# Kernel tuning notes

Measured on AMD Instinct MI355X. Metric: run time of the kernel, lower is better.

## Reference

```python
import jax, jax.numpy as jnp
import numpy as np

B, S, H = 1, 2048, 1024   # batch, seq_len, hidden_size
E, K, I = 8, 2, 1024      # num_experts, top_k, intermediate_size


def setup_inputs() -> dict:
    key = jax.random.key(0)
    ks = jax.random.split(key, 5)
    x = jax.random.normal(ks[0], (B, S, H), dtype=jnp.float32)
    gate_w = jax.random.normal(ks[1], (H, E), dtype=jnp.float32) * 0.02
    wg = jax.random.normal(ks[2], (E, H, I), dtype=jnp.float32) * 0.02  # gate_proj per expert
    wu = jax.random.normal(ks[3], (E, H, I), dtype=jnp.float32) * 0.02  # up_proj per expert
    wd = jax.random.normal(ks[4], (E, I, H), dtype=jnp.float32) * 0.02  # down_proj per expert
    return {"x": x, "gate_w": gate_w, "wg": wg, "wu": wu, "wd": wd}


def _moe(x, gate_w, wg, wu, wd):
    b, s, h = x.shape
    n = b * s
    logits = jnp.einsum('bsh,he->bse', x, gate_w)          # [B,S,E]
    top_vals, sel = jax.lax.top_k(logits, K)               # [B,S,K]
    rweights = jax.nn.softmax(top_vals, axis=-1)           # [B,S,K]
    x_flat = x.reshape(n, h)
    sel_flat = sel.reshape(n, K)
    rw_flat = rweights.reshape(n, K)

    def expert_body(out, params):
        e, Wg, Wu, Wd = params
        hit = jnp.any(sel_flat == e, axis=-1)              # [N] tokens routed to e in any slot
        # stable argsort: hit tokens first, in ascending original index order
        perm = jnp.argsort(jnp.logical_not(hit))
        tokens = x_flat[perm]                              # [N,H] (row j = j-th token of token_indices)
        y = jnp.einsum('ni,ih->nh', jax.nn.silu(tokens @ Wg) * (tokens @ Wu), Wd)  # [N,H]
        contrib = jnp.zeros_like(out)
        for k in range(K):
            km = sel_flat[:, k] == e                       # [N]
            # original does output_flat[k_indices] += w * expert_output[:len(k_indices)]
            # i.e. j-th token of k_indices gets expert_output row j
            ranks = jnp.clip(jnp.cumsum(km) - 1, 0, n - 1)
            w = jnp.where(km, rw_flat[:, k], 0.0)
            contrib = contrib + w[:, None] * y[ranks]
        return out + contrib, None

    out, _ = jax.lax.scan(expert_body, jnp.zeros_like(x_flat),
                          (jnp.arange(E), wg, wu, wd))
    output = out.reshape(b, s, h)

    # aux metrics (match LoadBalancedRouter)
    probs = jax.nn.softmax(logits, axis=-1)
    usage = probs.mean(axis=(0, 1))                        # [E]
    balance_loss = jnp.var(usage, ddof=1) * E              # torch.var is unbiased
    su = jnp.sort(usage)
    idx = jnp.arange(1, E + 1, dtype=usage.dtype)
    gini = 2.0 * (idx * su).sum() / (E * su.sum()) - (E + 1.0) / E
    entropy = -(probs * jnp.log(probs + 1e-10)).sum(-1).mean()
    return output, balance_loss, gini, entropy


def reference(x, gate_w, wg, wu, wd):
    return _moe(x, gate_w, wg, wu, wd)
```

## Files before the change

kernel.cpp:

```cpp
#include <hip/hip_runtime.h>
#include <stdint.h>

#define TOKENS 2048
#define HID 1024
#define NE 8

typedef __attribute__((ext_vector_type(8))) short bf16x8;
typedef __attribute__((ext_vector_type(4))) float f32x4;

__device__ __forceinline__ unsigned short f2bf(float f) {
  unsigned int u = __float_as_uint(f);
  return (unsigned short)((u + 0x7fffu + ((u >> 16) & 1u)) >> 16);
}

__device__ __forceinline__ void gload16(const void* g, void* l) {
  __builtin_amdgcn_global_load_lds((const __attribute__((address_space(1))) void*)g,
                                   (__attribute__((address_space(3))) void*)l, 16, 0, 0);
}

__global__ __launch_bounds__(256) void k_rout(
    const float* __restrict__ x, const float* __restrict__ gw,
    int* __restrict__ sel, float* __restrict__ rw,
    float* __restrict__ probs, float* __restrict__ ent) {
  const int w = threadIdx.x >> 6;
  const int lane = threadIdx.x & 63;
  const int t = blockIdx.x * 4 + w;

  const float4* x4 = (const float4*)(x + (size_t)t * HID);
  const float4* gw4 = (const float4*)gw;

  float acc[NE];
#pragma unroll
  for (int e = 0; e < NE; ++e) acc[e] = 0.f;

#pragma unroll
  for (int i = 0; i < 4; ++i) {
    const int idx4 = i * 64 + lane;
    const float4 xv = x4[idx4];
    float4 g[8];
#pragma unroll
    for (int k = 0; k < 8; ++k) g[k] = gw4[(size_t)idx4 * 8 + k];
    const float xs[4] = {xv.x, xv.y, xv.z, xv.w};
#pragma unroll
    for (int c = 0; c < 4; ++c) {
      acc[0] += xs[c] * g[c * 2].x;
      acc[1] += xs[c] * g[c * 2].y;
      acc[2] += xs[c] * g[c * 2].z;
      acc[3] += xs[c] * g[c * 2].w;
      acc[4] += xs[c] * g[c * 2 + 1].x;
      acc[5] += xs[c] * g[c * 2 + 1].y;
      acc[6] += xs[c] * g[c * 2 + 1].z;
      acc[7] += xs[c] * g[c * 2 + 1].w;
    }
  }

#pragma unroll
  for (int e = 0; e < NE; ++e) {
#pragma unroll
    for (int msk = 32; msk >= 1; msk >>= 1) acc[e] += __shfl_xor(acc[e], msk, 64);
  }

  float mx = acc[0];
#pragma unroll
  for (int e = 1; e < NE; ++e) mx = fmaxf(mx, acc[e]);

  const int e8 = lane & 7;
  float my = acc[0];
#pragma unroll
  for (int k = 1; k < NE; ++k) if (e8 == k) my = acc[k];
  const float exl = expf(my - mx);
  float S = exl;
#pragma unroll
  for (int msk = 1; msk <= 4; msk <<= 1) S += __shfl_xor(S, msk, 64);
  const float pp = exl / S;
  if (lane < 8) probs[t * NE + lane] = pp;
  float ev = -pp * logf(pp + 1e-10f);
#pragma unroll
  for (int msk = 1; msk <= 4; msk <<= 1) ev += __shfl_xor(ev, msk, 64);

  if (lane == 0) {
    ent[t] = ev;
    int b0 = 0; float v0 = acc[0];
#pragma unroll
    for (int e = 1; e < NE; ++e) if (acc[e] > v0) { v0 = acc[e]; b0 = e; }
    int b1 = -1; float v1 = 0.f;
#pragma unroll
    for (int e = 0; e < NE; ++e) {
      if (e != b0 && (b1 < 0 || acc[e] > v1)) { v1 = acc[e]; b1 = e; }
    }
    const float w1e = expf(v1 - v0);
    const float s2 = 1.f + w1e;
    sel[t * 2] = b0; sel[t * 2 + 1] = b1;
    rw[t * 2] = 1.f / s2; rw[t * 2 + 1] = w1e / s2;
  }
}

__global__ void k_metrics(const float* __restrict__ probs, const float* __restrict__ ent,
                          float* __restrict__ dout) {
  __shared__ float red[256][NE];
  __shared__ float rede[256];
  const int tid = threadIdx.x;
  const float4* p4 = (const float4*)probs;
  float pa[NE];
#pragma unroll
  for (int e = 0; e < NE; ++e) pa[e] = 0.f;
  float ea = 0.f;
  for (int t = tid; t < TOKENS; t += 256) {
    const float4 a = p4[t * 2];
    const float4 b = p4[t * 2 + 1];
    pa[0] += a.x; pa[1] += a.y; pa[2] += a.z; pa[3] += a.w;
    pa[4] += b.x; pa[5] += b.y; pa[6] += b.z; pa[7] += b.w;
    ea += ent[t];
  }
#pragma unroll
  for (int e = 0; e < NE; ++e) red[tid][e] = pa[e];
  rede[tid] = ea;
  __syncthreads();
  for (int s = 128; s >= 1; s >>= 1) {
    if (tid < s) {
#pragma unroll
      for (int e = 0; e < NE; ++e) red[tid][e] += red[tid + s][e];
      rede[tid] += rede[tid + s];
    }
    __syncthreads();
  }
  if (tid == 0) {
    float us[NE];
    for (int e = 0; e < NE; ++e) us[e] = red[0][e] / (float)TOKENS;
    float mean = 0.f;
    for (int e = 0; e < NE; ++e) mean += us[e];
    mean /= (float)NE;
    float var = 0.f;
    for (int e = 0; e < NE; ++e) { const float d = us[e] - mean; var += d * d; }
    var /= (float)(NE - 1);
    const float bl = var * (float)NE;
    for (int i = 1; i < NE; ++i) {
      const float key = us[i]; int j = i - 1;
      while (j >= 0 && us[j] > key) { us[j + 1] = us[j]; --j; }
      us[j + 1] = key;
    }
    float num = 0.f, den = 0.f;
    for (int i = 0; i < NE; ++i) { num += (float)(i + 1) * us[i]; den += us[i]; }
    const float gini = 2.f * num / ((float)NE * den) - (float)(NE + 1) / (float)NE;
    dout[(size_t)TOKENS * HID] = bl;
    dout[(size_t)TOKENS * HID + 1] = gini;
    dout[(size_t)TOKENS * HID + 2] = rede[0] / (float)TOKENS;
  }
}

__global__ void k_lists(const int* __restrict__ sel, int* __restrict__ cnt,
                        int* __restrict__ hit_list, int* __restrict__ rowidx) {
  const int e = blockIdx.x;
  const int tid = threadIdx.x;
  __shared__ unsigned long long ssum[256];
  __shared__ unsigned long long csumA[256];
  __shared__ unsigned long long csumB[256];

  int s0[8], s1[8];
  unsigned long long mine = 0ull;
  unsigned long long cA = 0ull, cB = 0ull;
#pragma unroll
  for (int j = 0; j < 8; ++j) {
    const int t = tid * 8 + j;
    s0[j] = sel[2 * t]; s1[j] = sel[2 * t + 1];
#pragma unroll
    for (int q = 0; q < 4; ++q) {
      cA += ((unsigned long long)((s0[j] == q) + (s1[j] == q))) << (16 * q);
      cB += ((unsigned long long)((s0[j] == q + 4) + (s1[j] == q + 4))) << (16 * q);
    }
    const unsigned long long k0 = (s0[j] == e) ? 1ull : 0ull;
    const unsigned long long k1 = (s1[j] == e) ? 1ull : 0ull;
    mine += (k0 | k1) | (k0 << 21) | (k1 << 42);
  }
  ssum[tid] = mine;
  csumA[tid] = cA;
  csumB[tid] = cB;
  __syncthreads();
  for (int s = 128; s >= 1; s >>= 1) {
    if (tid < s) { csumA[tid] += csumA[tid + s]; csumB[tid] += csumB[tid + s]; }
    __syncthreads();
  }
  const unsigned long long totA = csumA[0];
  const unsigned long long totB = csumB[0];
  int tc[NE];
#pragma unroll
  for (int q = 0; q < 4; ++q) {
    tc[q] = (int)((totA >> (16 * q)) & 0xFFFFull);
    tc[q + 4] = (int)((totB >> (16 * q)) & 0xFFFFull);
  }
  if (e == 0 && tid < NE) cnt[tid] = tc[tid];
  int poff = 0;
#pragma unroll
  for (int q = 0; q < NE; ++q) if (q < e) poff += (tc[q] + 127) & ~127;

  for (int s = 1; s < 256; s <<= 1) {
    const unsigned long long v = (tid >= s) ? ssum[tid - s] : 0ull;
    __syncthreads();
    ssum[tid] += v;
    __syncthreads();
  }
  const unsigned long long excl = (tid > 0) ? ssum[tid - 1] : 0ull;
  int hc = (int)(excl & 0x1FFFFFull);
  int c0 = (int)((excl >> 21) & 0x1FFFFFull);
  int c1 = (int)((excl >> 42) & 0x1FFFFFull);
#pragma unroll
  for (int j = 0; j < 8; ++j) {
    const int t = tid * 8 + j;
    const int k0 = (s0[j] == e), k1 = (s1[j] == e);
    if (k0 | k1) { hit_list[poff + hc] = t; ++hc; }
    if (k0) { rowidx[2 * t] = poff + c0; ++c0; }
    if (k1) { rowidx[2 * t + 1] = poff + c1; ++c1; }
  }
}

__global__ void k_tw(const float* __restrict__ wg, const float* __restrict__ wu,
                     const float* __restrict__ wd, unsigned short* __restrict__ wgt,
                     unsigned short* __restrict__ wut, unsigned short* __restrict__ wdt) {
  __shared__ float tile[64][65];
  const int bx = blockIdx.x;
  const int by = blockIdx.y;
  const int mi = blockIdx.z;
  const int tensor = mi >> 3, e = mi & 7;
  const float* src = (tensor == 0 ? wg : tensor == 1 ? wu : wd) + ((size_t)e << 20);
  unsigned short* dst = (tensor == 0 ? wgt : tensor == 1 ? wut : wdt) + ((size_t)e << 20);
  const int tid = threadIdx.x;
  const int tr = tid >> 4, tc = (tid & 15) * 4;
#pragma unroll
  for (int p = 0; p < 4; ++p) {
    const int row = p * 16 + tr;
    const float4 v = *(const float4*)(src + (size_t)(by * 64 + row) * 1024 + bx * 64 + tc);
    tile[row][tc] = v.x; tile[row][tc + 1] = v.y; tile[row][tc + 2] = v.z; tile[row][tc + 3] = v.w;
  }
  __syncthreads();
#pragma unroll
  for (int p = 0; p < 4; ++p) {
    const int row = p * 16 + tr;
    const ushort4 o = make_ushort4(f2bf(tile[tc + 0][row]), f2bf(tile[tc + 1][row]),
                                   f2bf(tile[tc + 2][row]), f2bf(tile[tc + 3][row]));
    *(ushort4*)(dst + (size_t)(bx * 64 + row) * 1024 + by * 64 + tc) = o;
  }
}

__global__ void k_gather(const float* __restrict__ x, const int* __restrict__ hit_list,
                         const int* __restrict__ cnt, unsigned short* __restrict__ A) {
  const int mb = blockIdx.x, e = blockIdx.y;
  const int ce = cnt[e];
  const int pc = (ce + 127) & ~127;
  if (mb * 8 >= pc) return;
  int poff = 0;
  for (int q = 0; q < e; ++q) poff += (cnt[q] + 127) & ~127;
  const int tid = threadIdx.x;
#pragma unroll
  for (int i = 0; i < 8; ++i) {
    const int rr = mb * 8 + i;
    unsigned short* dst = A + (size_t)(poff + rr) * 1024 + tid * 4;
    if (rr < ce) {
      const int t = hit_list[poff + rr];
      const float4 v = *(const float4*)(x + (size_t)t * 1024 + tid * 4);
      *(ushort4*)dst = make_ushort4(f2bf(v.x), f2bf(v.y), f2bf(v.z), f2bf(v.w));
    } else {
      *(ushort4*)dst = make_ushort4(0, 0, 0, 0);
    }
  }
}

__global__ __launch_bounds__(256, 4) void k_gemm1(
    const unsigned short* __restrict__ A, const unsigned short* __restrict__ wgt,
    const unsigned short* __restrict__ wut, const int* __restrict__ cnt,
    unsigned short* __restrict__ T) {
  const int nb = blockIdx.x, mb = blockIdx.y, e = blockIdx.z;
  const int ce = cnt[e];
  if (mb * 128 >= ce) return;
  int poff = 0;
  for (int q = 0; q < e; ++q) poff += (cnt[q] + 127) & ~127;

  const unsigned short* Ab = A + (size_t)(poff + mb * 128) * 1024;
  const unsigned short* Bg = wgt + ((size_t)e << 20) + ((size_t)nb << 16);
  const unsigned short* Bu = wut + ((size_t)e << 20) + ((size_t)nb << 16);

  __shared__ __align__(16) short lds[3][8192];

  const int tid = threadIdx.x;
  const int lane = tid & 63;
  const int w = tid >> 6;
  const int wm = w & 1, wn = w >> 1;
  const int r = lane & 15, gq = lane >> 4;
  const int slot = gq ^ ((r >> 1) & 3);
  const int srow = lane >> 2;
  const int skoff = ((lane & 3) ^ ((lane >> 3) & 3)) << 3;

  f32x4 accg[4][2], accu[4][2];
  const f32x4 fz = {0.f, 0.f, 0.f, 0.f};
#pragma unroll
  for (int i = 0; i < 4; ++i)
#pragma unroll
    for (int j = 0; j < 2; ++j) { accg[i][j] = fz; accu[i][j] = fz; }

  auto stage = [&](int kt, int b) {
#pragma unroll
    for (int q = 0; q < 4; ++q) {
      const int gseg = w + q * 4;
      const unsigned short* sb;
      int seg;
      if (gseg < 8) { sb = Ab; seg = gseg; }
      else if (gseg < 12) { sb = Bg; seg = gseg - 8; }
      else { sb = Bu; seg = gseg - 12; }
      gload16(sb + (size_t)(seg * 16 + srow) * 1024 + kt * 32 + skoff,
              &lds[b][gseg * 512]);
    }
  };

  stage(0, 0); stage(1, 1); stage(2, 2);
  int curb = 0;
  for (int kt = 0; kt < 32; ++kt) {
    if (kt < 30)      { asm volatile("s_waitcnt vmcnt(8)" ::: "memory"); }
    else if (kt == 30){ asm volatile("s_waitcnt vmcnt(4)" ::: "memory"); }
    else              { asm volatile("s_waitcnt vmcnt(0)" ::: "memory"); }
    __builtin_amdgcn_sched_barrier(0);
    __builtin_amdgcn_s_barrier();
    __builtin_amdgcn_sched_barrier(0);

    const short* La = &lds[curb][0];
    const short* Lg = &lds[curb][4096];
    const short* Lu = &lds[curb][6144];
    bf16x8 af[4], gf[2], uf[2];
#pragma unroll
    for (int f = 0; f < 4; ++f)
      af[f] = *(const bf16x8*)(La + (wm * 64 + f * 16 + r) * 32 + slot * 8);
#pragma unroll
    for (int f = 0; f < 2; ++f) {
      gf[f] = *(const bf16x8*)(Lg + (wn * 32 + f * 16 + r) * 32 + slot * 8);
      uf[f] = *(const bf16x8*)(Lu + (wn * 32 + f * 16 + r) * 32 + slot * 8);
    }
    asm volatile("s_waitcnt lgkmcnt(0)" ::: "memory");
    __builtin_amdgcn_sched_barrier(0);
    __builtin_amdgcn_s_barrier();
    __builtin_amdgcn_sched_barrier(0);
    if (kt <= 28) stage(kt + 3, curb);

#pragma unroll
    for (int i = 0; i < 4; ++i)
#pragma unroll
      for (int j = 0; j < 2; ++j) {
        accg[i][j] = __builtin_amdgcn_mfma_f32_16x16x32_bf16(af[i], gf[j], accg[i][j], 0, 0, 0);
        accu[i][j] = __builtin_amdgcn_mfma_f32_16x16x32_bf16(af[i], uf[j], accu[i][j], 0, 0, 0);
      }
    curb = (curb == 2) ? 0 : curb + 1;
  }

  const size_t rowbase = (size_t)(poff + mb * 128);
#pragma unroll
  for (int i = 0; i < 4; ++i)
#pragma unroll
    for (int j = 0; j < 2; ++j) {
      const int col = nb * 64 + wn * 32 + j * 16 + r;
#pragma unroll
      for (int rr = 0; rr < 4; ++rr) {
        const int rowt = wm * 64 + i * 16 + gq * 4 + rr;
        const float gv = accg[i][j][rr];
        const float uv = accu[i][j][rr];
        const float sv = gv / (1.f + expf(-gv)) * uv;
        T[(rowbase + rowt) * 1024 + col] = f2bf(sv);
      }
    }
}

__global__ __launch_bounds__(256, 4) void k_gemm2(
    const unsigned short* __restrict__ T, const unsigned short* __restrict__ wdt,
    const int* __restrict__ cnt, float* __restrict__ Y) {
  const int nb = blockIdx.x, mb = blockIdx.y, e = blockIdx.z;
  const int ce = cnt[e];
  if (mb * 128 >= ce) return;
  int poff = 0;
  for (int q = 0; q < e; ++q) poff += (cnt[q] + 127) & ~127;

  const unsigned short* Ab = T + (size_t)(poff + mb * 128) * 1024;
  const unsigned short* Bd = wdt + ((size_t)e << 20) + ((size_t)nb << 16);

  __shared__ __align__(16) short lds[3][6144];

  const int tid = threadIdx.x;
  const int lane = tid & 63;
  const int w = tid >> 6;
  const int wm = w & 1, wn = w >> 1;
  const int r = lane & 15, gq = lane >> 4;
  const int slot = gq ^ ((r >> 1) & 3);
  const int srow = lane >> 2;
  const int skoff = ((lane & 3) ^ ((lane >> 3) & 3)) << 3;

  f32x4 acc[4][2];
  const f32x4 fz = {0.f, 0.f, 0.f, 0.f};
#pragma unroll
  for (int i = 0; i < 4; ++i)
#pragma unroll
    for (int j = 0; j < 2; ++j) acc[i][j] = fz;

  auto stage = [&](int kt, int b) {
#pragma unroll
    for (int q = 0; q < 3; ++q) {
      const int gseg = w + q * 4;
      const unsigned short* sb;
      int seg;
      if (gseg < 8) { sb = Ab; seg = gseg; }
      else { sb = Bd; seg = gseg - 8; }
      gload16(sb + (size_t)(seg * 16 + srow) * 1024 + kt * 32 + skoff,
              &lds[b][gseg * 512]);
    }
  };

  stage(0, 0); stage(1, 1); stage(2, 2);
  int curb = 0;
  for (int kt = 0; kt < 32; ++kt) {
    if (kt < 30)      { asm volatile("s_waitcnt vmcnt(6)" ::: "memory"); }
    else if (kt == 30){ asm volatile("s_waitcnt vmcnt(3)" ::: "memory"); }
    else              { asm volatile("s_waitcnt vmcnt(0)" ::: "memory"); }
    __builtin_amdgcn_sched_barrier(0);
    __builtin_amdgcn_s_barrier();
    __builtin_amdgcn_sched_barrier(0);

    const short* La = &lds[curb][0];
    const short* Lb = &lds[curb][4096];
    bf16x8 af[4], bfr[2];
#pragma unroll
    for (int f = 0; f < 4; ++f)
      af[f] = *(const bf16x8*)(La + (wm * 64 + f * 16 + r) * 32 + slot * 8);
#pragma unroll
    for (int f = 0; f < 2; ++f)
      bfr[f] = *(const bf16x8*)(Lb + (wn * 32 + f * 16 + r) * 32 + slot * 8);
    asm volatile("s_waitcnt lgkmcnt(0)" ::: "memory");
    __builtin_amdgcn_sched_barrier(0);
    __builtin_amdgcn_s_barrier();
    __builtin_amdgcn_sched_barrier(0);
    if (kt <= 28) stage(kt + 3, curb);

#pragma unroll
    for (int i = 0; i < 4; ++i)
#pragma unroll
      for (int j = 0; j < 2; ++j)
        acc[i][j] = __builtin_amdgcn_mfma_f32_16x16x32_bf16(af[i], bfr[j], acc[i][j], 0, 0, 0);
    curb = (curb == 2) ? 0 : curb + 1;
  }

  const size_t rowbase = (size_t)(poff + mb * 128);
#pragma unroll
  for (int i = 0; i < 4; ++i)
#pragma unroll
    for (int j = 0; j < 2; ++j) {
      const int col = nb * 64 + wn * 32 + j * 16 + r;
#pragma unroll
      for (int rr = 0; rr < 4; ++rr) {
        const int rowt = wm * 64 + i * 16 + gq * 4 + rr;
        Y[(rowbase + rowt) * 1024 + col] = acc[i][j][rr];
      }
    }
}

__global__ void k_out(const float* __restrict__ Y, const int* __restrict__ rowidx,
                      const float* __restrict__ rw, float* __restrict__ out) {
  const int t = blockIdx.x;
  const int tid = threadIdx.x;
  const int r0 = rowidx[2 * t], r1 = rowidx[2 * t + 1];
  const float w0 = rw[2 * t], w1 = rw[2 * t + 1];
  const float4 y0 = *(const float4*)(Y + (size_t)r0 * HID + tid * 4);
  const float4 y1 = *(const float4*)(Y + (size_t)r1 * HID + tid * 4);
  float4 o;
  o.x = w0 * y0.x + w1 * y1.x;
  o.y = w0 * y0.y + w1 * y1.y;
  o.z = w0 * y0.z + w1 * y1.z;
  o.w = w0 * y0.w + w1 * y1.w;
  *(float4*)(out + (size_t)t * HID + tid * 4) = o;
}

extern "C" void kernel_launch(void* const* d_in, const int* in_sizes, int n_in,
                              void* d_out, int out_size, void* d_ws, size_t ws_size,
                              hipStream_t stream) {
  const float* x = (const float*)d_in[0];
  const float* gw = (const float*)d_in[1];
  const float* wg = (const float*)d_in[2];
  const float* wu = (const float*)d_in[3];
  const float* wd = (const float*)d_in[4];
  float* out = (float*)d_out;

  char* p = (char*)d_ws;
  unsigned short* wgt = (unsigned short*)p;
  unsigned short* wut = (unsigned short*)(p + 16777216);
  float* Y = (float*)p;
  unsigned short* wdt = (unsigned short*)(p + 33554432);
  unsigned short* A = (unsigned short*)(p + 50331648);
  unsigned short* T = (unsigned short*)(p + 60817408);
  char* q = p + 71303168;
  float* probs = (float*)q; q += 65536;
  float* ent = (float*)q; q += 8192;
  int* sel = (int*)q; q += 16384;
  float* rwp = (float*)q; q += 16384;
  int* rowidx = (int*)q; q += 16384;
  int* hit_list = (int*)q; q += 20480;
  int* cnt = (int*)q;

  k_rout<<<512, 256, 0, stream>>>(x, gw, sel, rwp, probs, ent);
  k_lists<<<8, 256, 0, stream>>>(sel, cnt, hit_list, rowidx);
  k_metrics<<<1, 256, 0, stream>>>(probs, ent, out);
  k_tw<<<dim3(16, 16, 24), 256, 0, stream>>>(wg, wu, wd, wgt, wut, wdt);
  k_gather<<<dim3(256, 8), 256, 0, stream>>>(x, hit_list, cnt, A);
  k_gemm1<<<dim3(16, 16, 8), 256, 0, stream>>>(A, wgt, wut, cnt, T);
  k_gemm2<<<dim3(16, 16, 8), 256, 0, stream>>>(T, wdt, cnt, Y);
  k_out<<<2048, 256, 0, stream>>>(Y, rowidx, rwp, out);
}
```

Before: 127.1 us.

## Fuse weight transpose and bf16 conversion into expert GEMM loaders

```diff
diff --git a/kernel.cpp b/kernel.cpp
--- a/kernel.cpp
+++ b/kernel.cpp
@@ -213,34 +213,6 @@
   }
 }
 
-__global__ void k_tw(const float* __restrict__ wg, const float* __restrict__ wu,
-                     const float* __restrict__ wd, unsigned short* __restrict__ wgt,
-                     unsigned short* __restrict__ wut, unsigned short* __restrict__ wdt) {
-  __shared__ float tile[64][65];
-  const int bx = blockIdx.x;
-  const int by = blockIdx.y;
-  const int mi = blockIdx.z;
-  const int tensor = mi >> 3, e = mi & 7;
-  const float* src = (tensor == 0 ? wg : tensor == 1 ? wu : wd) + ((size_t)e << 20);
-  unsigned short* dst = (tensor == 0 ? wgt : tensor == 1 ? wut : wdt) + ((size_t)e << 20);
-  const int tid = threadIdx.x;
-  const int tr = tid >> 4, tc = (tid & 15) * 4;
-#pragma unroll
-  for (int p = 0; p < 4; ++p) {
-    const int row = p * 16 + tr;
-    const float4 v = *(const float4*)(src + (size_t)(by * 64 + row) * 1024 + bx * 64 + tc);
-    tile[row][tc] = v.x; tile[row][tc + 1] = v.y; tile[row][tc + 2] = v.z; tile[row][tc + 3] = v.w;
-  }
-  __syncthreads();
-#pragma unroll
-  for (int p = 0; p < 4; ++p) {
-    const int row = p * 16 + tr;
-    const ushort4 o = make_ushort4(f2bf(tile[tc + 0][row]), f2bf(tile[tc + 1][row]),
-                                   f2bf(tile[tc + 2][row]), f2bf(tile[tc + 3][row]));
-    *(ushort4*)(dst + (size_t)(bx * 64 + row) * 1024 + by * 64 + tc) = o;
-  }
-}
-
 __global__ void k_gather(const float* __restrict__ x, const int* __restrict__ hit_list,
                          const int* __restrict__ cnt, unsigned short* __restrict__ A) {
   const int mb = blockIdx.x, e = blockIdx.y;
@@ -264,9 +236,9 @@
   }
 }
 
-__global__ __launch_bounds__(256, 4) void k_gemm1(
-    const unsigned short* __restrict__ A, const unsigned short* __restrict__ wgt,
-    const unsigned short* __restrict__ wut, const int* __restrict__ cnt,
+__global__ __launch_bounds__(256, 3) void k_gemm1(
+    const unsigned short* __restrict__ A, const float* __restrict__ wg,
+    const float* __restrict__ wu, const int* __restrict__ cnt,
     unsigned short* __restrict__ T) {
   const int nb = blockIdx.x, mb = blockIdx.y, e = blockIdx.z;
   const int ce = cnt[e];
@@ -275,8 +247,8 @@
   for (int q = 0; q < e; ++q) poff += (cnt[q] + 127) & ~127;
 
   const unsigned short* Ab = A + (size_t)(poff + mb * 128) * 1024;
-  const unsigned short* Bg = wgt + ((size_t)e << 20) + ((size_t)nb << 16);
-  const unsigned short* Bu = wut + ((size_t)e << 20) + ((size_t)nb << 16);
+  const float* Wg = wg + ((size_t)e << 20) + nb * 64;
+  const float* Wu = wu + ((size_t)e << 20) + nb * 64;
 
   __shared__ __align__(16) short lds[3][8192];
 
@@ -285,9 +257,11 @@
   const int w = tid >> 6;
   const int wm = w & 1, wn = w >> 1;
   const int r = lane & 15, gq = lane >> 4;
-  const int slot = gq ^ ((r >> 1) & 3);
+  const int aslot = gq ^ ((r >> 1) & 3);
+  const int wslot = gq ^ ((r >> 2) & 3);
   const int srow = lane >> 2;
   const int skoff = ((lane & 3) ^ ((lane >> 3) & 3)) << 3;
+  const int kp = tid >> 4, n4i = tid & 15;
 
   f32x4 accg[4][2], accu[4][2];
   const f32x4 fz = {0.f, 0.f, 0.f, 0.f};
@@ -296,48 +270,75 @@
 #pragma unroll
     for (int j = 0; j < 2; ++j) { accg[i][j] = fz; accu[i][j] = fz; }
 
-  auto stage = [&](int kt, int b) {
-#pragma unroll
-    for (int q = 0; q < 4; ++q) {
-      const int gseg = w + q * 4;
-      const unsigned short* sb;
-      int seg;
-      if (gseg < 8) { sb = Ab; seg = gseg; }
-      else if (gseg < 12) { sb = Bg; seg = gseg - 8; }
-      else { sb = Bu; seg = gseg - 12; }
-      gload16(sb + (size_t)(seg * 16 + srow) * 1024 + kt * 32 + skoff,
-              &lds[b][gseg * 512]);
-    }
-  };
-
-  stage(0, 0); stage(1, 1); stage(2, 2);
-  int curb = 0;
-  for (int kt = 0; kt < 32; ++kt) {
-    if (kt < 30)      { asm volatile("s_waitcnt vmcnt(8)" ::: "memory"); }
-    else if (kt == 30){ asm volatile("s_waitcnt vmcnt(4)" ::: "memory"); }
-    else              { asm volatile("s_waitcnt vmcnt(0)" ::: "memory"); }
-    __builtin_amdgcn_sched_barrier(0);
-    __builtin_amdgcn_s_barrier();
-    __builtin_amdgcn_sched_barrier(0);
-
+  auto stageA = [&](int kt, int b) {
+#pragma unroll
+    for (int q = 0; q < 2; ++q) {
+      const int seg = w + q * 4;
+      gload16(Ab + (size_t)(seg * 16 + srow) * 1024 + kt * 32 + skoff,
+              &lds[b][seg * 512]);
+    }
+  };
+  auto wload = [&](const float* W, int kt, float4& r0, float4& r1) {
+    const float* s = W + (size_t)(kt * 32 + 2 * kp) * 1024 + 4 * n4i;
+    r0 = *(const float4*)s;
+    r1 = *(const float4*)(s + 1024);
+  };
+  auto wwrite = [&](int b, int base, const float4& lo, const float4& hi) {
+    short* Lw = &lds[b][base];
+    const float l4[4] = {lo.x, lo.y, lo.z, lo.w};
+    const float h4[4] = {hi.x, hi.y, hi.z, hi.w};
+#pragma unroll
+    for (int j = 0; j < 4; ++j) {
+      unsigned int pk;
+      asm("v_cvt_pk_bf16_f32 %0, %1, %2" : "=v"(pk) : "v"(l4[j]), "v"(h4[j]));
+      const int n = 4 * n4i + j;
+      const int ps = (kp >> 2) ^ (n4i & 3);
+      *(unsigned int*)(Lw + n * 32 + ps * 8 + (kp & 3) * 2) = pk;
+    }
+  };
+
+  stageA(0, 0); stageA(1, 1); stageA(2, 2);
+  float4 g0A, g1A, u0A, u1A, g0B, g1B, u0B, u1B;
+  wload(Wg, 0, g0A, g1A); wload(Wu, 0, u0A, u1A);
+  wload(Wg, 1, g0B, g1B); wload(Wu, 1, u0B, u1B);
+  wwrite(0, 4096, g0A, g1A); wwrite(0, 6144, u0A, u1A);
+  wload(Wg, 2, g0A, g1A); wload(Wu, 2, u0A, u1A);
+  wwrite(1, 4096, g0B, g1B); wwrite(1, 6144, u0B, u1B);
+  asm volatile("s_waitcnt lgkmcnt(0)" ::: "memory");
+
+  auto iter = [&](int kt, float4& lg0, float4& lg1, float4& lu0, float4& lu1,
+                  const float4& sg0, const float4& sg1, const float4& su0, const float4& su1) {
+    asm volatile("s_waitcnt vmcnt(12)" ::: "memory");
+    __builtin_amdgcn_sched_barrier(0);
+    __builtin_amdgcn_s_barrier();
+    __builtin_amdgcn_sched_barrier(0);
+    const int curb = kt % 3;
     const short* La = &lds[curb][0];
     const short* Lg = &lds[curb][4096];
     const short* Lu = &lds[curb][6144];
     bf16x8 af[4], gf[2], uf[2];
 #pragma unroll
     for (int f = 0; f < 4; ++f)
-      af[f] = *(const bf16x8*)(La + (wm * 64 + f * 16 + r) * 32 + slot * 8);
+      af[f] = *(const bf16x8*)(La + (wm * 64 + f * 16 + r) * 32 + aslot * 8);
 #pragma unroll
     for (int f = 0; f < 2; ++f) {
-      gf[f] = *(const bf16x8*)(Lg + (wn * 32 + f * 16 + r) * 32 + slot * 8);
-      uf[f] = *(const bf16x8*)(Lu + (wn * 32 + f * 16 + r) * 32 + slot * 8);
+      gf[f] = *(const bf16x8*)(Lg + (wn * 32 + f * 16 + r) * 32 + wslot * 8);
+      uf[f] = *(const bf16x8*)(Lu + (wn * 32 + f * 16 + r) * 32 + wslot * 8);
     }
     asm volatile("s_waitcnt lgkmcnt(0)" ::: "memory");
     __builtin_amdgcn_sched_barrier(0);
     __builtin_amdgcn_s_barrier();
     __builtin_amdgcn_sched_barrier(0);
-    if (kt <= 28) stage(kt + 3, curb);
-
+    if (kt <= 28) {
+      wload(Wg, kt + 3, lg0, lg1);
+      wload(Wu, kt + 3, lu0, lu1);
+      stageA(kt + 3, curb);
+    }
+    if (kt <= 29) {
+      const int wb = (kt + 2) % 3;
+      wwrite(wb, 4096, sg0, sg1);
+      wwrite(wb, 6144, su0, su1);
+    }
 #pragma unroll
     for (int i = 0; i < 4; ++i)
 #pragma unroll
@@ -345,7 +346,43 @@
         accg[i][j] = __builtin_amdgcn_mfma_f32_16x16x32_bf16(af[i], gf[j], accg[i][j], 0, 0, 0);
         accu[i][j] = __builtin_amdgcn_mfma_f32_16x16x32_bf16(af[i], uf[j], accu[i][j], 0, 0, 0);
       }
-    curb = (curb == 2) ? 0 : curb + 1;
+  };
+
+  for (int k2 = 0; k2 < 15; ++k2) {
+    iter(2 * k2,     g0B, g1B, u0B, u1B, g0A, g1A, u0A, u1A);
+    iter(2 * k2 + 1, g0A, g1A, u0A, u1A, g0B, g1B, u0B, u1B);
+  }
+#pragma unroll
+  for (int kt = 30; kt < 32; ++kt) {
+    if (kt == 30) { asm volatile("s_waitcnt vmcnt(6)" ::: "memory"); }
+    else          { asm volatile("s_waitcnt vmcnt(0)" ::: "memory"); }
+    __builtin_amdgcn_sched_barrier(0);
+    __builtin_amdgcn_s_barrier();
+    __builtin_amdgcn_sched_barrier(0);
+    const int curb = kt % 3;
+    const short* La = &lds[curb][0];
+    const short* Lg = &lds[curb][4096];
+    const short* Lu = &lds[curb][6144];
+    bf16x8 af[4], gf[2], uf[2];
+#pragma unroll
+    for (int f = 0; f < 4; ++f)
+      af[f] = *(const bf16x8*)(La + (wm * 64 + f * 16 + r) * 32 + aslot * 8);
+#pragma unroll
+    for (int f = 0; f < 2; ++f) {
+      gf[f] = *(const bf16x8*)(Lg + (wn * 32 + f * 16 + r) * 32 + wslot * 8);
+      uf[f] = *(const bf16x8*)(Lu + (wn * 32 + f * 16 + r) * 32 + wslot * 8);
+    }
+    asm volatile("s_waitcnt lgkmcnt(0)" ::: "memory");
+    __builtin_amdgcn_sched_barrier(0);
+    __builtin_amdgcn_s_barrier();
+    __builtin_amdgcn_sched_barrier(0);
+#pragma unroll
+    for (int i = 0; i < 4; ++i)
+#pragma unroll
+      for (int j = 0; j < 2; ++j) {
+        accg[i][j] = __builtin_amdgcn_mfma_f32_16x16x32_bf16(af[i], gf[j], accg[i][j], 0, 0, 0);
+        accu[i][j] = __builtin_amdgcn_mfma_f32_16x16x32_bf16(af[i], uf[j], accu[i][j], 0, 0, 0);
+      }
   }
 
   const size_t rowbase = (size_t)(poff + mb * 128);
@@ -366,7 +403,7 @@
 }
 
 __global__ __launch_bounds__(256, 4) void k_gemm2(
-    const unsigned short* __restrict__ T, const unsigned short* __restrict__ wdt,
+    const unsigned short* __restrict__ T, const float* __restrict__ wd,
     const int* __restrict__ cnt, float* __restrict__ Y) {
   const int nb = blockIdx.x, mb = blockIdx.y, e = blockIdx.z;
   const int ce = cnt[e];
@@ -375,7 +412,7 @@
   for (int q = 0; q < e; ++q) poff += (cnt[q] + 127) & ~127;
 
   const unsigned short* Ab = T + (size_t)(poff + mb * 128) * 1024;
-  const unsigned short* Bd = wdt + ((size_t)e << 20) + ((size_t)nb << 16);
+  const float* Wd = wd + ((size_t)e << 20) + nb * 64;
 
   __shared__ __align__(16) short lds[3][6144];
 
@@ -384,9 +421,11 @@
   const int w = tid >> 6;
   const int wm = w & 1, wn = w >> 1;
   const int r = lane & 15, gq = lane >> 4;
-  const int slot = gq ^ ((r >> 1) & 3);
+  const int aslot = gq ^ ((r >> 1) & 3);
+  const int wslot = gq ^ ((r >> 2) & 3);
   const int srow = lane >> 2;
   const int skoff = ((lane & 3) ^ ((lane >> 3) & 3)) << 3;
+  const int kp = tid >> 4, n4i = tid & 15;
 
   f32x4 acc[4][2];
   const f32x4 fz = {0.f, 0.f, 0.f, 0.f};
@@ -395,50 +434,105 @@
 #pragma unroll
     for (int j = 0; j < 2; ++j) acc[i][j] = fz;
 
-  auto stage = [&](int kt, int b) {
-#pragma unroll
-    for (int q = 0; q < 3; ++q) {
-      const int gseg = w + q * 4;
-      const unsigned short* sb;
-      int seg;
-      if (gseg < 8) { sb = Ab; seg = gseg; }
-      else { sb = Bd; seg = gseg - 8; }
-      gload16(sb + (size_t)(seg * 16 + srow) * 1024 + kt * 32 + skoff,
-              &lds[b][gseg * 512]);
-    }
-  };
-
-  stage(0, 0); stage(1, 1); stage(2, 2);
-  int curb = 0;
-  for (int kt = 0; kt < 32; ++kt) {
-    if (kt < 30)      { asm volatile("s_waitcnt vmcnt(6)" ::: "memory"); }
-    else if (kt == 30){ asm volatile("s_waitcnt vmcnt(3)" ::: "memory"); }
-    else              { asm volatile("s_waitcnt vmcnt(0)" ::: "memory"); }
-    __builtin_amdgcn_sched_barrier(0);
-    __builtin_amdgcn_s_barrier();
-    __builtin_amdgcn_sched_barrier(0);
-
+  auto stageA = [&](int kt, int b) {
+#pragma unroll
+    for (int q = 0; q < 2; ++q) {
+      const int seg = w + q * 4;
+      gload16(Ab + (size_t)(seg * 16 + srow) * 1024 + kt * 32 + skoff,
+              &lds[b][seg * 512]);
+    }
+  };
+  auto wload = [&](int kt, float4& r0, float4& r1) {
+    const float* s = Wd + (size_t)(kt * 32 + 2 * kp) * 1024 + 4 * n4i;
+    r0 = *(const float4*)s;
+    r1 = *(const float4*)(s + 1024);
+  };
+  auto wwrite = [&](int b, const float4& lo, const float4& hi) {
+    short* Lw = &lds[b][4096];
+    const float l4[4] = {lo.x, lo.y, lo.z, lo.w};
+    const float h4[4] = {hi.x, hi.y, hi.z, hi.w};
+#pragma unroll
+    for (int j = 0; j < 4; ++j) {
+      unsigned int pk;
+      asm("v_cvt_pk_bf16_f32 %0, %1, %2" : "=v"(pk) : "v"(l4[j]), "v"(h4[j]));
+      const int n = 4 * n4i + j;
+      const int ps = (kp >> 2) ^ (n4i & 3);
+      *(unsigned int*)(Lw + n * 32 + ps * 8 + (kp & 3) * 2) = pk;
+    }
+  };
+
+  stageA(0, 0); stageA(1, 1); stageA(2, 2);
+  float4 d0A, d1A, d0B, d1B;
+  wload(0, d0A, d1A);
+  wload(1, d0B, d1B);
+  wwrite(0, d0A, d1A);
+  wload(2, d0A, d1A);
+  wwrite(1, d0B, d1B);
+  asm volatile("s_waitcnt lgkmcnt(0)" ::: "memory");
+
+  auto iter = [&](int kt, float4& l0, float4& l1, const float4& s0, const float4& s1) {
+    asm volatile("s_waitcnt vmcnt(8)" ::: "memory");
+    __builtin_amdgcn_sched_barrier(0);
+    __builtin_amdgcn_s_barrier();
+    __builtin_amdgcn_sched_barrier(0);
+    const int curb = kt % 3;
     const short* La = &lds[curb][0];
     const short* Lb = &lds[curb][4096];
     bf16x8 af[4], bfr[2];
 #pragma unroll
     for (int f = 0; f < 4; ++f)
-      af[f] = *(const bf16x8*)(La + (wm * 64 + f * 16 + r) * 32 + slot * 8);
+      af[f] = *(const bf16x8*)(La + (wm * 64 + f * 16 + r) * 32 + aslot * 8);
 #pragma unroll
     for (int f = 0; f < 2; ++f)
-      bfr[f] = *(const bf16x8*)(Lb + (wn * 32 + f * 16 + r) * 32 + slot * 8);
+      bfr[f] = *(const bf16x8*)(Lb + (wn * 32 + f * 16 + r) * 32 + wslot * 8);
     asm volatile("s_waitcnt lgkmcnt(0)" ::: "memory");
     __builtin_amdgcn_sched_barrier(0);
     __builtin_amdgcn_s_barrier();
     __builtin_amdgcn_sched_barrier(0);
-    if (kt <= 28) stage(kt + 3, curb);
-
+    if (kt <= 28) {
+      wload(kt + 3, l0, l1);
+      stageA(kt + 3, curb);
+    }
+    if (kt <= 29) {
+      wwrite((kt + 2) % 3, s0, s1);
+    }
 #pragma unroll
     for (int i = 0; i < 4; ++i)
 #pragma unroll
       for (int j = 0; j < 2; ++j)
         acc[i][j] = __builtin_amdgcn_mfma_f32_16x16x32_bf16(af[i], bfr[j], acc[i][j], 0, 0, 0);
-    curb = (curb == 2) ? 0 : curb + 1;
+  };
+
+  for (int k2 = 0; k2 < 15; ++k2) {
+    iter(2 * k2,     d0B, d1B, d0A, d1A);
+    iter(2 * k2 + 1, d0A, d1A, d0B, d1B);
+  }
+#pragma unroll
+  for (int kt = 30; kt < 32; ++kt) {
+    if (kt == 30) { asm volatile("s_waitcnt vmcnt(4)" ::: "memory"); }
+    else          { asm volatile("s_waitcnt vmcnt(0)" ::: "memory"); }
+    __builtin_amdgcn_sched_barrier(0);
+    __builtin_amdgcn_s_barrier();
+    __builtin_amdgcn_sched_barrier(0);
+    const int curb = kt % 3;
+    const short* La = &lds[curb][0];
+    const short* Lb = &lds[curb][4096];
+    bf16x8 af[4], bfr[2];
+#pragma unroll
+    for (int f = 0; f < 4; ++f)
+      af[f] = *(const bf16x8*)(La + (wm * 64 + f * 16 + r) * 32 + aslot * 8);
+#pragma unroll
+    for (int f = 0; f < 2; ++f)
+      bfr[f] = *(const bf16x8*)(Lb + (wn * 32 + f * 16 + r) * 32 + wslot * 8);
+    asm volatile("s_waitcnt lgkmcnt(0)" ::: "memory");
+    __builtin_amdgcn_sched_barrier(0);
+    __builtin_amdgcn_s_barrier();
+    __builtin_amdgcn_sched_barrier(0);
+#pragma unroll
+    for (int i = 0; i < 4; ++i)
+#pragma unroll
+      for (int j = 0; j < 2; ++j)
+        acc[i][j] = __builtin_amdgcn_mfma_f32_16x16x32_bf16(af[i], bfr[j], acc[i][j], 0, 0, 0);
   }
 
   const size_t rowbase = (size_t)(poff + mb * 128);
@@ -482,13 +576,10 @@
   float* out = (float*)d_out;
 
   char* p = (char*)d_ws;
-  unsigned short* wgt = (unsigned short*)p;
-  unsigned short* wut = (unsigned short*)(p + 16777216);
-  float* Y = (float*)p;
-  unsigned short* wdt = (unsigned short*)(p + 33554432);
-  unsigned short* A = (unsigned short*)(p + 50331648);
-  unsigned short* T = (unsigned short*)(p + 60817408);
-  char* q = p + 71303168;
+  unsigned short* A = (unsigned short*)p;
+  unsigned short* T = (unsigned short*)(p + 12582912);
+  float* Y = (float*)(p + 25165824);
+  char* q = p + 48234496;
   float* probs = (float*)q; q += 65536;
   float* ent = (float*)q; q += 8192;
   int* sel = (int*)q; q += 16384;
@@ -500,9 +591,8 @@
   k_rout<<<512, 256, 0, stream>>>(x, gw, sel, rwp, probs, ent);
   k_lists<<<8, 256, 0, stream>>>(sel, cnt, hit_list, rowidx);
   k_metrics<<<1, 256, 0, stream>>>(probs, ent, out);
-  k_tw<<<dim3(16, 16, 24), 256, 0, stream>>>(wg, wu, wd, wgt, wut, wdt);
   k_gather<<<dim3(256, 8), 256, 0, stream>>>(x, hit_list, cnt, A);
-  k_gemm1<<<dim3(16, 16, 8), 256, 0, stream>>>(A, wgt, wut, cnt, T);
-  k_gemm2<<<dim3(16, 16, 8), 256, 0, stream>>>(T, wdt, cnt, Y);
+  k_gemm1<<<dim3(16, 16, 8), 256, 0, stream>>>(A, wg, wu, cnt, T);
+  k_gemm2<<<dim3(16, 16, 8), 256, 0, stream>>>(T, wd, cnt, Y);
   k_out<<<2048, 256, 0, stream>>>(Y, rowidx, rwp, out);
 }
```

Measured after the change: 116.2 us. -8.6%, faster.

## Fuse wd bf16 conversion into down-proj GEMM and merge small pre-kernels

Applied to the files above, without the earlier changes.

```diff
diff --git a/kernel.cpp b/kernel.cpp
--- a/kernel.cpp
+++ b/kernel.cpp
@@ -18,13 +18,44 @@
                                    (__attribute__((address_space(3))) void*)l, 16, 0, 0);
 }
 
-__global__ __launch_bounds__(256) void k_rout(
+__global__ __launch_bounds__(256) void k_pre(
     const float* __restrict__ x, const float* __restrict__ gw,
+    const float* __restrict__ wg, const float* __restrict__ wu,
+    unsigned short* __restrict__ wgt, unsigned short* __restrict__ wut,
     int* __restrict__ sel, float* __restrict__ rw,
     float* __restrict__ probs, float* __restrict__ ent) {
-  const int w = threadIdx.x >> 6;
-  const int lane = threadIdx.x & 63;
-  const int t = blockIdx.x * 4 + w;
+  __shared__ float tile[64][65];
+  const int bid = blockIdx.x;
+  const int tid = threadIdx.x;
+
+  if (bid < 4096) {
+    const int bx = bid & 15;
+    const int by = (bid >> 4) & 15;
+    const int e = (bid >> 8) & 7;
+    const int tensor = (bid >> 11) & 1;
+    const float* src = (tensor == 0 ? wg : wu) + ((size_t)e << 20);
+    unsigned short* dst = (tensor == 0 ? wgt : wut) + ((size_t)e << 20);
+    const int tr = tid >> 4, tc = (tid & 15) * 4;
+#pragma unroll
+    for (int p = 0; p < 4; ++p) {
+      const int row = p * 16 + tr;
+      const float4 v = *(const float4*)(src + (size_t)(by * 64 + row) * 1024 + bx * 64 + tc);
+      tile[row][tc] = v.x; tile[row][tc + 1] = v.y; tile[row][tc + 2] = v.z; tile[row][tc + 3] = v.w;
+    }
+    __syncthreads();
+#pragma unroll
+    for (int p = 0; p < 4; ++p) {
+      const int row = p * 16 + tr;
+      const ushort4 o = make_ushort4(f2bf(tile[tc + 0][row]), f2bf(tile[tc + 1][row]),
+                                     f2bf(tile[tc + 2][row]), f2bf(tile[tc + 3][row]));
+      *(ushort4*)(dst + (size_t)(bx * 64 + row) * 1024 + by * 64 + tc) = o;
+    }
+    return;
+  }
+
+  const int w = tid >> 6;
+  const int lane = tid & 63;
+  const int t = (bid - 4096) * 4 + w;
 
   const float4* x4 = (const float4*)(x + (size_t)t * HID);
   const float4* gw4 = (const float4*)gw;
@@ -95,63 +126,65 @@
   }
 }
 
-__global__ void k_metrics(const float* __restrict__ probs, const float* __restrict__ ent,
-                          float* __restrict__ dout) {
-  __shared__ float red[256][NE];
-  __shared__ float rede[256];
+__global__ void k_aux(const int* __restrict__ sel, int* __restrict__ cnt,
+                      int* __restrict__ hit_list, int* __restrict__ rowidx,
+                      const float* __restrict__ probs, const float* __restrict__ ent,
+                      float* __restrict__ dout) {
   const int tid = threadIdx.x;
-  const float4* p4 = (const float4*)probs;
-  float pa[NE];
-#pragma unroll
-  for (int e = 0; e < NE; ++e) pa[e] = 0.f;
-  float ea = 0.f;
-  for (int t = tid; t < TOKENS; t += 256) {
-    const float4 a = p4[t * 2];
-    const float4 b = p4[t * 2 + 1];
-    pa[0] += a.x; pa[1] += a.y; pa[2] += a.z; pa[3] += a.w;
-    pa[4] += b.x; pa[5] += b.y; pa[6] += b.z; pa[7] += b.w;
-    ea += ent[t];
-  }
-#pragma unroll
-  for (int e = 0; e < NE; ++e) red[tid][e] = pa[e];
-  rede[tid] = ea;
-  __syncthreads();
-  for (int s = 128; s >= 1; s >>= 1) {
-    if (tid < s) {
-#pragma unroll
-      for (int e = 0; e < NE; ++e) red[tid][e] += red[tid + s][e];
-      rede[tid] += rede[tid + s];
-    }
+
+  if (blockIdx.x == 8) {
+    __shared__ float red[256][NE];
+    __shared__ float rede[256];
+    const float4* p4 = (const float4*)probs;
+    float pa[NE];
+#pragma unroll
+    for (int e = 0; e < NE; ++e) pa[e] = 0.f;
+    float ea = 0.f;
+    for (int t = tid; t < TOKENS; t += 256) {
+      const float4 a = p4[t * 2];
+      const float4 b = p4[t * 2 + 1];
+      pa[0] += a.x; pa[1] += a.y; pa[2] += a.z; pa[3] += a.w;
+      pa[4] += b.x; pa[5] += b.y; pa[6] += b.z; pa[7] += b.w;
+      ea += ent[t];
+    }
+#pragma unroll
+    for (int e = 0; e < NE; ++e) red[tid][e] = pa[e];
+    rede[tid] = ea;
     __syncthreads();
-  }
-  if (tid == 0) {
-    float us[NE];
-    for (int e = 0; e < NE; ++e) us[e] = red[0][e] / (float)TOKENS;
-    float mean = 0.f;
-    for (int e = 0; e < NE; ++e) mean += us[e];
-    mean /= (float)NE;
-    float var = 0.f;
-    for (int e = 0; e < NE; ++e) { const float d = us[e] - mean; var += d * d; }
-    var /= (float)(NE - 1);
-    const float bl = var * (float)NE;
-    for (int i = 1; i < NE; ++i) {
-      const float key = us[i]; int j = i - 1;
-      while (j >= 0 && us[j] > key) { us[j + 1] = us[j]; --j; }
-      us[j + 1] = key;
-    }
-    float num = 0.f, den = 0.f;
-    for (int i = 0; i < NE; ++i) { num += (float)(i + 1) * us[i]; den += us[i]; }
-    const float gini = 2.f * num / ((float)NE * den) - (float)(NE + 1) / (float)NE;
-    dout[(size_t)TOKENS * HID] = bl;
-    dout[(size_t)TOKENS * HID + 1] = gini;
-    dout[(size_t)TOKENS * HID + 2] = rede[0] / (float)TOKENS;
-  }
-}
-
-__global__ void k_lists(const int* __restrict__ sel, int* __restrict__ cnt,
-                        int* __restrict__ hit_list, int* __restrict__ rowidx) {
+    for (int s = 128; s >= 1; s >>= 1) {
+      if (tid < s) {
+#pragma unroll
+        for (int e = 0; e < NE; ++e) red[tid][e] += red[tid + s][e];
+        rede[tid] += rede[tid + s];
+      }
+      __syncthreads();
+    }
+    if (tid == 0) {
+      float us[NE];
+      for (int e = 0; e < NE; ++e) us[e] = red[0][e] / (float)TOKENS;
+      float mean = 0.f;
+      for (int e = 0; e < NE; ++e) mean += us[e];
+      mean /= (float)NE;
+      float var = 0.f;
+      for (int e = 0; e < NE; ++e) { const float d = us[e] - mean; var += d * d; }
+      var /= (float)(NE - 1);
+      const float bl = var * (float)NE;
+      for (int i = 1; i < NE; ++i) {
+        const float key = us[i]; int j = i - 1;
+        while (j >= 0 && us[j] > key) { us[j + 1] = us[j]; --j; }
+        us[j + 1] = key;
+      }
+      float num = 0.f, den = 0.f;
+      for (int i = 0; i < NE; ++i) { num += (float)(i + 1) * us[i]; den += us[i]; }
+      const float gini = 2.f * num / ((float)NE * den) - (float)(NE + 1) / (float)NE;
+      dout[(size_t)TOKENS * HID] = bl;
+      dout[(size_t)TOKENS * HID + 1] = gini;
+      dout[(size_t)TOKENS * HID + 2] = rede[0] / (float)TOKENS;
+    }
+    return;
+  }
+
   const int e = blockIdx.x;
-  const int tid = threadIdx.x;
   __shared__ unsigned long long ssum[256];
   __shared__ unsigned long long csumA[256];
   __shared__ unsigned long long csumB[256];
@@ -210,34 +243,6 @@
     if (k0 | k1) { hit_list[poff + hc] = t; ++hc; }
     if (k0) { rowidx[2 * t] = poff + c0; ++c0; }
     if (k1) { rowidx[2 * t + 1] = poff + c1; ++c1; }
-  }
-}
-
-__global__ void k_tw(const float* __restrict__ wg, const float* __restrict__ wu,
-                     const float* __restrict__ wd, unsigned short* __restrict__ wgt,
-                     unsigned short* __restrict__ wut, unsigned short* __restrict__ wdt) {
-  __shared__ float tile[64][65];
-  const int bx = blockIdx.x;
-  const int by = blockIdx.y;
-  const int mi = blockIdx.z;
-  const int tensor = mi >> 3, e = mi & 7;
-  const float* src = (tensor == 0 ? wg : tensor == 1 ? wu : wd) + ((size_t)e << 20);
-  unsigned short* dst = (tensor == 0 ? wgt : tensor == 1 ? wut : wdt) + ((size_t)e << 20);
-  const int tid = threadIdx.x;
-  const int tr = tid >> 4, tc = (tid & 15) * 4;
-#pragma unroll
-  for (int p = 0; p < 4; ++p) {
-    const int row = p * 16 + tr;
-    const float4 v = *(const float4*)(src + (size_t)(by * 64 + row) * 1024 + bx * 64 + tc);
-    tile[row][tc] = v.x; tile[row][tc + 1] = v.y; tile[row][tc + 2] = v.z; tile[row][tc + 3] = v.w;
-  }
-  __syncthreads();
-#pragma unroll
-  for (int p = 0; p < 4; ++p) {
-    const int row = p * 16 + tr;
-    const ushort4 o = make_ushort4(f2bf(tile[tc + 0][row]), f2bf(tile[tc + 1][row]),
-                                   f2bf(tile[tc + 2][row]), f2bf(tile[tc + 3][row]));
-    *(ushort4*)(dst + (size_t)(bx * 64 + row) * 1024 + by * 64 + tc) = o;
   }
 }
 
@@ -366,7 +371,7 @@
 }
 
 __global__ __launch_bounds__(256, 4) void k_gemm2(
-    const unsigned short* __restrict__ T, const unsigned short* __restrict__ wdt,
+    const unsigned short* __restrict__ T, const float* __restrict__ wd,
     const int* __restrict__ cnt, float* __restrict__ Y) {
   const int nb = blockIdx.x, mb = blockIdx.y, e = blockIdx.z;
   const int ce = cnt[e];
@@ -375,7 +380,7 @@
   for (int q = 0; q < e; ++q) poff += (cnt[q] + 127) & ~127;
 
   const unsigned short* Ab = T + (size_t)(poff + mb * 128) * 1024;
-  const unsigned short* Bd = wdt + ((size_t)e << 20) + ((size_t)nb << 16);
+  const float* Wd = wd + ((size_t)e << 20) + nb * 64;
 
   __shared__ __align__(16) short lds[3][6144];
 
@@ -384,9 +389,11 @@
   const int w = tid >> 6;
   const int wm = w & 1, wn = w >> 1;
   const int r = lane & 15, gq = lane >> 4;
-  const int slot = gq ^ ((r >> 1) & 3);
+  const int aslot = gq ^ ((r >> 1) & 3);
   const int srow = lane >> 2;
   const int skoff = ((lane & 3) ^ ((lane >> 3) & 3)) << 3;
+  const int wn_ = tid & 63, wkoct = tid >> 6;
+  const int wps = wkoct ^ ((wn_ >> 1) & 3);
 
   f32x4 acc[4][2];
   const f32x4 fz = {0.f, 0.f, 0.f, 0.f};
@@ -395,50 +402,98 @@
 #pragma unroll
     for (int j = 0; j < 2; ++j) acc[i][j] = fz;
 
-  auto stage = [&](int kt, int b) {
-#pragma unroll
-    for (int q = 0; q < 3; ++q) {
-      const int gseg = w + q * 4;
-      const unsigned short* sb;
-      int seg;
-      if (gseg < 8) { sb = Ab; seg = gseg; }
-      else { sb = Bd; seg = gseg - 8; }
-      gload16(sb + (size_t)(seg * 16 + srow) * 1024 + kt * 32 + skoff,
-              &lds[b][gseg * 512]);
+  auto stageA = [&](int kt, int b) {
+#pragma unroll
+    for (int q = 0; q < 2; ++q) {
+      const int seg = w + q * 4;
+      gload16(Ab + (size_t)(seg * 16 + srow) * 1024 + kt * 32 + skoff,
+              &lds[b][seg * 512]);
     }
   };
-
-  stage(0, 0); stage(1, 1); stage(2, 2);
-  int curb = 0;
-  for (int kt = 0; kt < 32; ++kt) {
-    if (kt < 30)      { asm volatile("s_waitcnt vmcnt(6)" ::: "memory"); }
-    else if (kt == 30){ asm volatile("s_waitcnt vmcnt(3)" ::: "memory"); }
-    else              { asm volatile("s_waitcnt vmcnt(0)" ::: "memory"); }
+  auto wload = [&](int kt, float* f) {
+    const float* s = Wd + (size_t)(kt * 32 + wkoct * 8) * 1024 + wn_;
+#pragma unroll
+    for (int i = 0; i < 8; ++i) f[i] = s[i * 1024];
+  };
+  auto wwrite = [&](int b, const float* f) {
+    unsigned int pk[4];
+#pragma unroll
+    for (int j = 0; j < 4; ++j)
+      asm("v_cvt_pk_bf16_f32 %0, %1, %2" : "=v"(pk[j]) : "v"(f[2 * j]), "v"(f[2 * j + 1]));
+    *(uint4*)((char*)&lds[b][4096] + wn_ * 64 + wps * 16) =
+        make_uint4(pk[0], pk[1], pk[2], pk[3]);
+  };
+
+  stageA(0, 0); stageA(1, 1); stageA(2, 2);
+  float dA[8], dB[8];
+  wload(0, dA);
+  wload(1, dB);
+  wwrite(0, dA);
+  wload(2, dA);
+  wwrite(1, dB);
+  asm volatile("s_waitcnt lgkmcnt(0)" ::: "memory");
+
+  auto iter = [&](int kt, float* l, const float* s) {
+    asm volatile("s_waitcnt vmcnt(20)" ::: "memory");
     __builtin_amdgcn_sched_barrier(0);
     __builtin_amdgcn_s_barrier();
     __builtin_amdgcn_sched_barrier(0);
-
+    const int curb = kt % 3;
     const short* La = &lds[curb][0];
     const short* Lb = &lds[curb][4096];
     bf16x8 af[4], bfr[2];
 #pragma unroll
     for (int f = 0; f < 4; ++f)
-      af[f] = *(const bf16x8*)(La + (wm * 64 + f * 16 + r) * 32 + slot * 8);
+      af[f] = *(const bf16x8*)(La + (wm * 64 + f * 16 + r) * 32 + aslot * 8);
 #pragma unroll
     for (int f = 0; f < 2; ++f)
-      bfr[f] = *(const bf16x8*)(Lb + (wn * 32 + f * 16 + r) * 32 + slot * 8);
+      bfr[f] = *(const bf16x8*)(Lb + (wn * 32 + f * 16 + r) * 32 + aslot * 8);
     asm volatile("s_waitcnt lgkmcnt(0)" ::: "memory");
     __builtin_amdgcn_sched_barrier(0);
     __builtin_amdgcn_s_barrier();
     __builtin_amdgcn_sched_barrier(0);
-    if (kt <= 28) stage(kt + 3, curb);
-
+    if (kt <= 28) {
+      wload(kt + 3, l);
+      stageA(kt + 3, curb);
+    }
 #pragma unroll
     for (int i = 0; i < 4; ++i)
 #pragma unroll
       for (int j = 0; j < 2; ++j)
         acc[i][j] = __builtin_amdgcn_mfma_f32_16x16x32_bf16(af[i], bfr[j], acc[i][j], 0, 0, 0);
-    curb = (curb == 2) ? 0 : curb + 1;
+    if (kt <= 29) wwrite((kt + 2) % 3, s);
+  };
+
+  for (int k2 = 0; k2 < 15; ++k2) {
+    iter(2 * k2,     dB, dA);
+    iter(2 * k2 + 1, dA, dB);
+  }
+#pragma unroll
+  for (int kt = 30; kt < 32; ++kt) {
+    if (kt == 30) { asm volatile("s_waitcnt vmcnt(10)" ::: "memory"); }
+    else          { asm volatile("s_waitcnt vmcnt(0)" ::: "memory"); }
+    __builtin_amdgcn_sched_barrier(0);
+    __builtin_amdgcn_s_barrier();
+    __builtin_amdgcn_sched_barrier(0);
+    const int curb = kt % 3;
+    const short* La = &lds[curb][0];
+    const short* Lb = &lds[curb][4096];
+    bf16x8 af[4], bfr[2];
+#pragma unroll
+    for (int f = 0; f < 4; ++f)
+      af[f] = *(const bf16x8*)(La + (wm * 64 + f * 16 + r) * 32 + aslot * 8);
+#pragma unroll
+    for (int f = 0; f < 2; ++f)
+      bfr[f] = *(const bf16x8*)(Lb + (wn * 32 + f * 16 + r) * 32 + aslot * 8);
+    asm volatile("s_waitcnt lgkmcnt(0)" ::: "memory");
+    __builtin_amdgcn_sched_barrier(0);
+    __builtin_amdgcn_s_barrier();
+    __builtin_amdgcn_sched_barrier(0);
+#pragma unroll
+    for (int i = 0; i < 4; ++i)
+#pragma unroll
+      for (int j = 0; j < 2; ++j)
+        acc[i][j] = __builtin_amdgcn_mfma_f32_16x16x32_bf16(af[i], bfr[j], acc[i][j], 0, 0, 0);
   }
 
   const size_t rowbase = (size_t)(poff + mb * 128);
@@ -485,10 +540,9 @@
   unsigned short* wgt = (unsigned short*)p;
   unsigned short* wut = (unsigned short*)(p + 16777216);
   float* Y = (float*)p;
-  unsigned short* wdt = (unsigned short*)(p + 33554432);
-  unsigned short* A = (unsigned short*)(p + 50331648);
-  unsigned short* T = (unsigned short*)(p + 60817408);
-  char* q = p + 71303168;
+  unsigned short* A = (unsigned short*)(p + 33554432);
+  unsigned short* T = (unsigned short*)(p + 46137344);
+  char* q = p + 58720256;
   float* probs = (float*)q; q += 65536;
   float* ent = (float*)q; q += 8192;
   int* sel = (int*)q; q += 16384;
@@ -497,12 +551,10 @@
   int* hit_list = (int*)q; q += 20480;
   int* cnt = (int*)q;
 
-  k_rout<<<512, 256, 0, stream>>>(x, gw, sel, rwp, probs, ent);
-  k_lists<<<8, 256, 0, stream>>>(sel, cnt, hit_list, rowidx);
-  k_metrics<<<1, 256, 0, stream>>>(probs, ent, out);
-  k_tw<<<dim3(16, 16, 24), 256, 0, stream>>>(wg, wu, wd, wgt, wut, wdt);
+  k_pre<<<4608, 256, 0, stream>>>(x, gw, wg, wu, wgt, wut, sel, rwp, probs, ent);
+  k_aux<<<9, 256, 0, stream>>>(sel, cnt, hit_list, rowidx, probs, ent, out);
   k_gather<<<dim3(256, 8), 256, 0, stream>>>(x, hit_list, cnt, A);
   k_gemm1<<<dim3(16, 16, 8), 256, 0, stream>>>(A, wgt, wut, cnt, T);
-  k_gemm2<<<dim3(16, 16, 8), 256, 0, stream>>>(T, wdt, cnt, Y);
+  k_gemm2<<<dim3(16, 16, 8), 256, 0, stream>>>(T, wd, cnt, Y);
   k_out<<<2048, 256, 0, stream>>>(Y, rowidx, rwp, out);
 }
```

New measurement: 122.3 us. 3.8% less time.
